# Performance work log

Hardware: AMD Instinct MI355X
Metric: run time of the kernel (lower is better)

The kernel has to match this reference:

```python
import jax, jax.numpy as jnp
import numpy as np

# dims
N = 50000      # total nodes in merged batch graph
M = 250000     # edges for GNN propagation
E = 200000     # candidate edges scored by mixture-Bernoulli head
MAXN = 512     # max_num_nodes (padded adjacency row length)
H = 128        # hidden_dim = embedding_dim = msg_dim
EF = 128       # edge_feat_dim = 2 * att_edge_dim
ATT = 128      # att_hidden_dim
K = 20         # num_mix_component
L = 3          # num_GNN_layers
S = 512        # num_subgraph
B = 16         # batch of graphs
C = 1          # num_canonical_order


def setup_inputs() -> dict:
    key = jax.random.key(0)
    ks = list(jax.random.split(key, 64))
    it = iter(ks)
    nk = lambda: next(it)
    d = {}
    d['node_feat'] = jax.random.normal(nk(), (N, MAXN), jnp.float32)
    d['edge'] = jax.random.randint(nk(), (M, 2), 0, N, dtype=jnp.int32)
    d['edge_feat'] = jax.random.normal(nk(), (M, EF), jnp.float32)
    d['node_idx_gnn'] = jax.random.randint(nk(), (E, 2), 0, N, dtype=jnp.int32)
    d['label'] = (jax.random.uniform(nk(), (E,)) < 0.1).astype(jnp.float32)
    # even sorted partition of E candidate edges into S subgraphs (all nonempty)
    d['subgraph_idx'] = ((jnp.arange(E) * S) // E).astype(jnp.int32)
    # bc_idx = repeat_interleave(arange(B*C), subgraphs_per_graph)
    d['bc_idx'] = jnp.repeat(jnp.arange(B * C, dtype=jnp.int32), S // (B * C))
    # params
    def lin(k, out_d, in_d):
        return jax.random.normal(k, (out_d, in_d), jnp.float32) * (1.0 / np.sqrt(in_d))
    d['dec_W'] = lin(nk(), H, MAXN); d['dec_b'] = jnp.zeros((H,), jnp.float32)
    d['msg_W1'] = jnp.stack([lin(nk(), H, H + EF) for _ in range(L)])
    d['msg_b1'] = jnp.zeros((L, H), jnp.float32)
    d['msg_W2'] = jnp.stack([lin(nk(), H, H) for _ in range(L)])
    d['msg_b2'] = jnp.zeros((L, H), jnp.float32)
    d['att_W1'] = jnp.stack([lin(nk(), ATT, H + EF) for _ in range(L)])
    d['att_b1'] = jnp.zeros((L, ATT), jnp.float32)
    d['att_W2'] = jnp.stack([lin(nk(), H, ATT) for _ in range(L)])
    d['att_b2'] = jnp.zeros((L, H), jnp.float32)
    d['gru_Wih'] = jnp.stack([lin(nk(), 3 * H, H) for _ in range(L)])
    d['gru_bih'] = jnp.zeros((L, 3 * H), jnp.float32)
    d['gru_Whh'] = jnp.stack([lin(nk(), 3 * H, H) for _ in range(L)])
    d['gru_bhh'] = jnp.zeros((L, 3 * H), jnp.float32)
    d['th_W1'] = lin(nk(), H, H); d['th_b1'] = jnp.zeros((H,), jnp.float32)
    d['th_W2'] = lin(nk(), H, H); d['th_b2'] = jnp.zeros((H,), jnp.float32)
    d['th_W3'] = lin(nk(), K, H); d['th_b3'] = jnp.zeros((K,), jnp.float32)
    d['al_W1'] = lin(nk(), H, H); d['al_b1'] = jnp.zeros((H,), jnp.float32)
    d['al_W2'] = lin(nk(), H, H); d['al_b2'] = jnp.zeros((H,), jnp.float32)
    d['al_W3'] = lin(nk(), K, H); d['al_b3'] = jnp.zeros((K,), jnp.float32)
    return d


def _gran_forward(node_feat, edge_feat, label, dec_W, dec_b, msg_W1, msg_b1,
                  msg_W2, msg_b2, att_W1, att_b1, att_W2, att_b2, gru_Wih,
                  gru_bih, gru_Whh, gru_bhh, th_W1, th_b1, th_W2, th_b2,
                  th_W3, th_b3, al_W1, al_b1, al_W2, al_b2, al_W3, al_b3,
                  edge, node_idx_gnn, subgraph_idx, bc_idx):
    n = node_feat.shape[0]
    # decoder_input: Linear(max_num_nodes -> embedding_dim)
    state = node_feat @ dec_W.T + dec_b  # [N, H]
    src, dst = edge[:, 0], edge[:, 1]
    for l in range(L):
        if l > 0:
            state = jax.nn.relu(state)
        # _prop: gather diff, msg MLP, sigmoid attention gate, scatter-sum, GRU
        diff = state[src] - state[dst]                       # [M, H]
        ei = jnp.concatenate([diff, edge_feat], axis=1)      # [M, H+EF]
        msg = jax.nn.relu(ei @ msg_W1[l].T + msg_b1[l]) @ msg_W2[l].T + msg_b2[l]
        att = jax.nn.sigmoid(jax.nn.relu(ei @ att_W1[l].T + att_b1[l]) @ att_W2[l].T + att_b2[l])
        agg = jax.ops.segment_sum(msg * att, dst, num_segments=n)  # [N, H]
        # torch GRUCell
        gi = agg @ gru_Wih[l].T + gru_bih[l]
        gh = state @ gru_Whh[l].T + gru_bhh[l]
        i_r, i_z, i_n = jnp.split(gi, 3, axis=-1)
        h_r, h_z, h_n = jnp.split(gh, 3, axis=-1)
        r = jax.nn.sigmoid(i_r + h_r)
        z = jax.nn.sigmoid(i_z + h_z)
        nn_ = jnp.tanh(i_n + r * h_n)
        state = (1.0 - z) * nn_ + z * state
    # mixture-Bernoulli heads on candidate-edge node-state diffs
    d2 = state[node_idx_gnn[:, 0]] - state[node_idx_gnn[:, 1]]  # [E, H]
    def mlp3(x, W1, b1, W2, b2, W3, b3):
        h = jax.nn.relu(x @ W1.T + b1)
        h = jax.nn.relu(h @ W2.T + b2)
        return h @ W3.T + b3
    log_theta = mlp3(d2, th_W1, th_b1, th_W2, th_b2, th_W3, th_b3)  # [E, K]
    log_alpha = mlp3(d2, al_W1, al_b1, al_W2, al_b2, al_W3, al_b3)  # [E, K]
    # mixture_bernoulli_loss (pos_weight = 1.0)
    y = label[:, None]
    adj_loss = jax.nn.softplus(-log_theta) + (1.0 - y) * log_theta  # BCEWithLogits, [E, K]
    const = jax.ops.segment_sum(jnp.ones((label.shape[0],), log_theta.dtype), subgraph_idx, num_segments=S)
    reduce_adj = jax.ops.segment_sum(adj_loss, subgraph_idx, num_segments=S)     # [S, K]
    reduce_la = jax.ops.segment_sum(log_alpha, subgraph_idx, num_segments=S)
    reduce_la = jax.nn.log_softmax(reduce_la / const[:, None], axis=-1)
    log_prob = jax.scipy.special.logsumexp(-reduce_adj + reduce_la, axis=1)      # [S]
    bc_log_prob = jax.ops.segment_sum(log_prob, bc_idx, num_segments=B * C)
    bc_const = jax.ops.segment_sum(const, bc_idx, num_segments=B * C)
    bc_loss = (bc_log_prob / bc_const).reshape(B, C)
    b_loss = jax.scipy.special.logsumexp(bc_loss, axis=1)  # logsumexp over orderings
    return jnp.mean(-b_loss)


def reference(node_feat, edge, edge_feat, node_idx_gnn, label, subgraph_idx,
              bc_idx, dec_W, dec_b, msg_W1, msg_b1, msg_W2, msg_b2, att_W1,
              att_b1, att_W2, att_b2, gru_Wih, gru_bih, gru_Whh, gru_bhh,
              th_W1, th_b1, th_W2, th_b2, th_W3, th_b3, al_W1, al_b1, al_W2,
              al_b2, al_W3, al_b3):
    return _gran_forward(node_feat, edge_feat, label, dec_W, dec_b, msg_W1,
                         msg_b1, msg_W2, msg_b2, att_W1, att_b1, att_W2,
                         att_b2, gru_Wih, gru_bih, gru_Whh, gru_bhh, th_W1,
                         th_b1, th_W2, th_b2, th_W3, th_b3, al_W1, al_b1,
                         al_W2, al_b2, al_W3, al_b3, edge, node_idx_gnn,
                         subgraph_idx, bc_idx)
```

## Files before the change

### kernel.cpp

```cpp
#include <hip/hip_runtime.h>
#include <cstdint>
#include <cstddef>


typedef __bf16 bf16x8 __attribute__((ext_vector_type(8)));
typedef short  s16x8  __attribute__((ext_vector_type(8)));
typedef short  s16x4  __attribute__((ext_vector_type(4)));
typedef float  f32x4  __attribute__((ext_vector_type(4)));

__device__ inline unsigned short f2bf(float f) {
    return __builtin_bit_cast(unsigned short, (__bf16)f);
}
__device__ inline float bf2f(unsigned short b) {
    return __uint_as_float(((unsigned int)b) << 16);
}
__device__ inline unsigned int pk2(float a, float b) {
    return ((unsigned int)f2bf(b) << 16) | f2bf(a);
}
__device__ inline f32x4 MFMA(bf16x8 a, bf16x8 b, f32x4 c) {
    return __builtin_amdgcn_mfma_f32_16x16x32_bf16(a, b, c, 0, 0, 0);
}

__device__ inline bf16x8 ld_swz(const char* lds, int row, int unit) {
    return *(const bf16x8*)(lds + row * 256 + ((unit ^ (row & 7)) << 4));
}
__device__ inline void hid_write(char* HID, int h0, int erow, s16x4 s4) {
    int unit = h0 >> 3;
    *(s16x4*)(HID + erow * 256 + ((unit ^ (erow & 7)) << 4) + ((h0 & 4) << 1)) = s4;
}
__device__ inline bf16x8 ldA(const short* __restrict__ Wb, int K, int row, int koff) {
    return *(const bf16x8*)(Wb + (size_t)row * K + koff);
}
__device__ inline bf16x8 ld_f32_frag(const float* __restrict__ p) {
    float4 a = *(const float4*)p, b = *(const float4*)(p + 4);
    s16x8 s;
    s[0] = f2bf(a.x); s[1] = f2bf(a.y); s[2] = f2bf(a.z); s[3] = f2bf(a.w);
    s[4] = f2bf(b.x); s[5] = f2bf(b.y); s[6] = f2bf(b.z); s[7] = f2bf(b.w);
    return __builtin_bit_cast(bf16x8, s);
}

#define NPACK 31
struct PrepackArgs {
    const float* src[NPACK];
    short*       dst[NPACK];
    int stride[NPACK];
    int rows[NPACK];
    int rowsTot[NPACK];
    int cols[NPACK];
};

__global__ void prepack(PrepackArgs a) {
    int e = blockIdx.y;
    int row = blockIdx.x;
    if (row >= a.rowsTot[e]) return;
    int c8 = threadIdx.x;
    if (c8 * 8 >= a.cols[e]) return;
    s16x8 s = {};
    if (row < a.rows[e]) {
        const float* p = a.src[e] + (size_t)row * a.stride[e] + c8 * 8;
        float4 x = *(const float4*)p, y = *(const float4*)(p + 4);
        s[0] = f2bf(x.x); s[1] = f2bf(x.y); s[2] = f2bf(x.z); s[3] = f2bf(x.w);
        s[4] = f2bf(y.x); s[5] = f2bf(y.y); s[6] = f2bf(y.z); s[7] = f2bf(y.w);
    }
    *(s16x8*)(a.dst[e] + (size_t)row * a.cols[e] + c8 * 8) = s;
}

__device__ inline void proj_gemm_store(const char* ST, char* PJ,
                                       const short* __restrict__ projW,
                                       short* __restrict__ proj,
                                       int rb, int R, int tid)
{
    const int l = tid & 63, w = tid >> 6;
    f32x4 accP[2][2][4] = {};
#pragma unroll
    for (int ks = 0; ks < 4; ++ks) {
        int koff = ks * 32 + (l >> 4) * 8;
        bf16x8 aw[2][2];
#pragma unroll
        for (int pc = 0; pc < 2; ++pc)
#pragma unroll
            for (int mt = 0; mt < 2; ++mt)
                aw[pc][mt] = ldA(projW, 128, pc * 128 + 32 * w + 16 * mt + (l & 15), koff);
#pragma unroll
        for (int n = 0; n < 4; ++n) {
            bf16x8 b = ld_swz(ST, 16 * n + (l & 15), ks * 4 + (l >> 4));
#pragma unroll
            for (int pc = 0; pc < 2; ++pc)
#pragma unroll
                for (int mt = 0; mt < 2; ++mt)
                    accP[pc][mt][n] = MFMA(aw[pc][mt], b, accP[pc][mt][n]);
        }
    }
    const int half = w >> 1;
#pragma unroll
    for (int hh = 0; hh < 2; ++hh) {
        __syncthreads();
        if (half == hh) {
#pragma unroll
            for (int pc = 0; pc < 2; ++pc)
#pragma unroll
                for (int mt = 0; mt < 2; ++mt) {
                    int h0 = 32 * w + 16 * mt + ((l >> 4) << 2);
                    int colp = 2 * h0 + 4 * pc - 128 * hh;
#pragma unroll
                    for (int n = 0; n < 4; ++n) {
                        f32x4 v = accP[pc][mt][n];
                        s16x4 s4;
                        s4[0] = f2bf(v[0]); s4[1] = f2bf(v[1]);
                        s4[2] = f2bf(v[2]); s4[3] = f2bf(v[3]);
                        hid_write(PJ, colp, 16 * n + (l & 15), s4);
                    }
                }
        }
        __syncthreads();
#pragma unroll
        for (int p2 = 0; p2 < 4; ++p2) {
            int row = p2 * 16 + (tid >> 4);
            int r = rb + row;
            if (r < R) {
                bf16x8 v = ld_swz(PJ, row, tid & 15);
                *(s16x8*)(proj + (size_t)r * 256 + hh * 128 + (tid & 15) * 8) =
                    __builtin_bit_cast(s16x8, v);
            }
        }
    }
}

__global__ __launch_bounds__(256, 3)
void dec_proj(const float* __restrict__ nf, int R,
              const short* __restrict__ decWb, const float* __restrict__ bias,
              const short* __restrict__ projW,
              short* __restrict__ sOut, short* __restrict__ proj)
{
    __shared__ char ST[16384];
    __shared__ char PJ[16384];
    const int tid = threadIdx.x, l = tid & 63, w = tid >> 6;
    const int rb = blockIdx.x * 64;

    const float* brow[4];
#pragma unroll
    for (int n = 0; n < 4; ++n) {
        int row = rb + 16 * n + (l & 15); if (row >= R) row = R - 1;
        brow[n] = nf + (size_t)row * 512;
    }

    f32x4 acc[2][4] = {};
    for (int kc = 0; kc < 512; kc += 128) {
#pragma unroll
        for (int ks = 0; ks < 4; ++ks) {
            int koff = kc + ks * 32 + (l >> 4) * 8;
            bf16x8 a0 = ldA(decWb, 512, 32 * w + (l & 15), koff);
            bf16x8 a1 = ldA(decWb, 512, 32 * w + 16 + (l & 15), koff);
#pragma unroll
            for (int n = 0; n < 4; ++n) {
                bf16x8 b = ld_f32_frag(brow[n] + koff);
                acc[0][n] = MFMA(a0, b, acc[0][n]);
                acc[1][n] = MFMA(a1, b, acc[1][n]);
            }
        }
    }
#pragma unroll
    for (int mt = 0; mt < 2; ++mt) {
        int c0 = 32 * w + 16 * mt + ((l >> 4) << 2);
        float4 bv = *(const float4*)&bias[c0];
#pragma unroll
        for (int n = 0; n < 4; ++n) {
            f32x4 v = acc[mt][n];
            s16x4 s4;
            s4[0] = f2bf(v[0] + bv.x); s4[1] = f2bf(v[1] + bv.y);
            s4[2] = f2bf(v[2] + bv.z); s4[3] = f2bf(v[3] + bv.w);
            hid_write(ST, c0, 16 * n + (l & 15), s4);
        }
    }
    __syncthreads();
#pragma unroll
    for (int p2 = 0; p2 < 4; ++p2) {
        int row = p2 * 16 + (tid >> 4);
        int r = rb + row;
        if (r < R) {
            bf16x8 v = ld_swz(ST, row, tid & 15);
            *(s16x8*)(sOut + (size_t)r * 128 + (tid & 15) * 8) =
                __builtin_bit_cast(s16x8, v);
        }
    }
    proj_gemm_store(ST, PJ, projW, proj, rb, R, tid);
}

template<int HAS_PROJ>
__global__ __launch_bounds__(256, 2)
void node_fused(const short* __restrict__ aggb, const short* __restrict__ sin_,
                const short* __restrict__ Wih, const short* __restrict__ Whh,
                const float* __restrict__ bih, const float* __restrict__ bhh,
                const short* __restrict__ projW,
                short* __restrict__ sOut, short* __restrict__ proj, int R)
{
    __shared__ char ST[16384];
    __shared__ char PJ[16384];
    const int tid = threadIdx.x, l = tid & 63, w = tid >> 6;
    const int rb = blockIdx.x * 64;

    const short* arow[4];
    const short* srow[4];
#pragma unroll
    for (int n = 0; n < 4; ++n) {
        int row = rb + 16 * n + (l & 15); if (row >= R) row = R - 1;
        arow[n] = aggb + (size_t)row * 128;
        srow[n] = sin_ + (size_t)row * 128;
    }
    s16x4 svv[2][4];
#pragma unroll
    for (int mt = 0; mt < 2; ++mt) {
        int c0 = 32 * w + 16 * mt + ((l >> 4) << 2);
#pragma unroll
        for (int n = 0; n < 4; ++n)
            svv[mt][n] = *(const s16x4*)(srow[n] + c0);
    }

    unsigned int rpk[2][4][2], zpk[2][4][2];

    for (int p = 0; p < 3; ++p) {
        f32x4 gia[2][4] = {}, gha[2][4] = {};
#pragma unroll
        for (int ks = 0; ks < 4; ++ks) {
            int koff = ks * 32 + (l >> 4) * 8;
            bf16x8 ai0 = ldA(Wih, 128, p * 128 + 32 * w + (l & 15), koff);
            bf16x8 ai1 = ldA(Wih, 128, p * 128 + 32 * w + 16 + (l & 15), koff);
            bf16x8 ah0 = ldA(Whh, 128, p * 128 + 32 * w + (l & 15), koff);
            bf16x8 ah1 = ldA(Whh, 128, p * 128 + 32 * w + 16 + (l & 15), koff);
#pragma unroll
            for (int n = 0; n < 4; ++n) {
                bf16x8 ba = *(const bf16x8*)(arow[n] + koff);
                bf16x8 bs = *(const bf16x8*)(srow[n] + koff);
                gia[0][n] = MFMA(ai0, ba, gia[0][n]);
                gia[1][n] = MFMA(ai1, ba, gia[1][n]);
                gha[0][n] = MFMA(ah0, bs, gha[0][n]);
                gha[1][n] = MFMA(ah1, bs, gha[1][n]);
            }
        }
#pragma unroll
        for (int mt = 0; mt < 2; ++mt) {
            int c0 = 32 * w + 16 * mt + ((l >> 4) << 2);
            float4 bi = *(const float4*)&bih[p * 128 + c0];
            float4 bh = *(const float4*)&bhh[p * 128 + c0];
            float biv[4] = {bi.x, bi.y, bi.z, bi.w};
            float bhv[4] = {bh.x, bh.y, bh.z, bh.w};
#pragma unroll
            for (int n = 0; n < 4; ++n) {
                float gv[4], hv[4];
#pragma unroll
                for (int q = 0; q < 4; ++q) {
                    gv[q] = gia[mt][n][q] + biv[q];
                    hv[q] = gha[mt][n][q] + bhv[q];
                }
                if (p == 0) {
                    rpk[mt][n][0] = pk2(1.f / (1.f + expf(-(gv[0] + hv[0]))),
                                        1.f / (1.f + expf(-(gv[1] + hv[1]))));
                    rpk[mt][n][1] = pk2(1.f / (1.f + expf(-(gv[2] + hv[2]))),
                                        1.f / (1.f + expf(-(gv[3] + hv[3]))));
                } else if (p == 1) {
                    zpk[mt][n][0] = pk2(1.f / (1.f + expf(-(gv[0] + hv[0]))),
                                        1.f / (1.f + expf(-(gv[1] + hv[1]))));
                    zpk[mt][n][1] = pk2(1.f / (1.f + expf(-(gv[2] + hv[2]))),
                                        1.f / (1.f + expf(-(gv[3] + hv[3]))));
                } else {
                    s16x4 s4;
#pragma unroll
                    for (int q = 0; q < 4; ++q) {
                        unsigned int ru = rpk[mt][n][q >> 1], zu = zpk[mt][n][q >> 1];
                        float r = bf2f((unsigned short)((q & 1) ? (ru >> 16) : (ru & 0xffffu)));
                        float z = bf2f((unsigned short)((q & 1) ? (zu >> 16) : (zu & 0xffffu)));
                        float nn = tanhf(gv[q] + r * hv[q]);
                        float o = (1.f - z) * nn + z * bf2f((unsigned short)svv[mt][n][q]);
                        s4[q] = f2bf(HAS_PROJ ? fmaxf(o, 0.f) : o);
                    }
                    hid_write(ST, c0, 16 * n + (l & 15), s4);
                }
            }
        }
    }
    __syncthreads();
#pragma unroll
    for (int p2 = 0; p2 < 4; ++p2) {
        int row = p2 * 16 + (tid >> 4);
        int r = rb + row;
        if (r < R) {
            bf16x8 v = ld_swz(ST, row, tid & 15);
            *(s16x8*)(sOut + (size_t)r * 128 + (tid & 15) * 8) =
                __builtin_bit_cast(s16x8, v);
        }
    }
    if (HAS_PROJ)
        proj_gemm_store(ST, PJ, projW, proj, rb, R, tid);
}

__global__ __launch_bounds__(256, 3)
void edge_fused2(const short* __restrict__ efc,
                 const int* __restrict__ srcs, const int* __restrict__ dsts,
                 const short* __restrict__ proj,
                 const short* __restrict__ mW1b, const short* __restrict__ mW2,
                 const short* __restrict__ aW1b, const short* __restrict__ aW2,
                 const float* __restrict__ mb1, const float* __restrict__ mb2,
                 const float* __restrict__ ab1, const float* __restrict__ ab2,
                 short* __restrict__ msgatt, int M, int ntiles)
{
    __shared__ char HIDm[16384];
    __shared__ char HIDa[16384];
    const int tid = threadIdx.x, l = tid & 63, w = tid >> 6;
    int q = ntiles >> 3, r = ntiles & 7;
    int xcd = blockIdx.x & 7, o = blockIdx.x >> 3;
    int tile = (xcd < r ? xcd * (q + 1) : r * (q + 1) + (xcd - r) * q) + o;
    const int pb = tile * 64;

    const char* erow[4];
    int dstv[4];
    s16x8 psv[2][4];
    {
#pragma unroll
        for (int n = 0; n < 4; ++n) {
            int pos = pb + 16 * n + (l & 15); if (pos >= M) pos = M - 1;
            int sv = srcs[pos];
            dstv[n] = dsts[pos];
            erow[n] = (const char*)(efc + (size_t)pos * 128);
#pragma unroll
            for (int mt = 0; mt < 2; ++mt) {
                int off = 2 * (32 * w + 16 * mt + ((l >> 4) << 2));
                psv[mt][n] = *(const s16x8*)(proj + (size_t)sv * 256 + off);
            }
        }
    }

    f32x4 accm[2][4] = {}, acca[2][4] = {};
#pragma unroll
    for (int ks = 0; ks < 4; ++ks) {
        int koff = ks * 32 + (l >> 4) * 8;
        bf16x8 am0 = ldA(mW1b, 128, 32 * w + (l & 15), koff);
        bf16x8 am1 = ldA(mW1b, 128, 32 * w + 16 + (l & 15), koff);
        bf16x8 aa0 = ldA(aW1b, 128, 32 * w + (l & 15), koff);
        bf16x8 aa1 = ldA(aW1b, 128, 32 * w + 16 + (l & 15), koff);
#pragma unroll
        for (int n = 0; n < 4; ++n) {
            bf16x8 b = *(const bf16x8*)(erow[n] + koff * 2);
            accm[0][n] = MFMA(am0, b, accm[0][n]);
            accm[1][n] = MFMA(am1, b, accm[1][n]);
            acca[0][n] = MFMA(aa0, b, acca[0][n]);
            acca[1][n] = MFMA(aa1, b, acca[1][n]);
        }
    }
#pragma unroll
    for (int mt = 0; mt < 2; ++mt) {
        int h0 = 32 * w + 16 * mt + ((l >> 4) << 2);
        float4 bm = *(const float4*)&mb1[h0];
        float4 ba = *(const float4*)&ab1[h0];
        float bmv[4] = {bm.x, bm.y, bm.z, bm.w};
        float bav[4] = {ba.x, ba.y, ba.z, ba.w};
#pragma unroll
        for (int n = 0; n < 4; ++n) {
            s16x8 ps = psv[mt][n];
            s16x8 pd = *(const s16x8*)(proj + (size_t)dstv[n] * 256 + 2 * h0);
            f32x4 vm = accm[mt][n], va = acca[mt][n];
            s16x4 sm, sa;
#pragma unroll
            for (int qq = 0; qq < 4; ++qq) {
                float m_ = vm[qq] + bmv[qq] + bf2f((unsigned short)ps[qq])
                           - bf2f((unsigned short)pd[qq]);
                float a_ = va[qq] + bav[qq] + bf2f((unsigned short)ps[qq + 4])
                           - bf2f((unsigned short)pd[qq + 4]);
                sm[qq] = f2bf(fmaxf(m_, 0.f));
                sa[qq] = f2bf(fmaxf(a_, 0.f));
            }
            hid_write(HIDm, h0, 16 * n + (l & 15), sm);
            hid_write(HIDa, h0, 16 * n + (l & 15), sa);
        }
    }
    __syncthreads();

    f32x4 acc2m[2][4] = {}, acc2a[2][4] = {};
#pragma unroll
    for (int ks = 0; ks < 4; ++ks) {
        int koff = ks * 32 + (l >> 4) * 8;
        bf16x8 wm0 = ldA(mW2, 128, 32 * w + (l & 15), koff);
        bf16x8 wm1 = ldA(mW2, 128, 32 * w + 16 + (l & 15), koff);
        bf16x8 wa0 = ldA(aW2, 128, 32 * w + (l & 15), koff);
        bf16x8 wa1 = ldA(aW2, 128, 32 * w + 16 + (l & 15), koff);
#pragma unroll
        for (int n = 0; n < 4; ++n) {
            bf16x8 bm = ld_swz(HIDm, 16 * n + (l & 15), ks * 4 + (l >> 4));
            bf16x8 ba = ld_swz(HIDa, 16 * n + (l & 15), ks * 4 + (l >> 4));
            acc2m[0][n] = MFMA(wm0, bm, acc2m[0][n]);
            acc2m[1][n] = MFMA(wm1, bm, acc2m[1][n]);
            acc2a[0][n] = MFMA(wa0, ba, acc2a[0][n]);
            acc2a[1][n] = MFMA(wa1, ba, acc2a[1][n]);
        }
    }
    __syncthreads();
#pragma unroll
    for (int mt = 0; mt < 2; ++mt) {
        int c0 = 32 * w + 16 * mt + ((l >> 4) << 2);
        float4 bm2 = *(const float4*)&mb2[c0];
        float4 ba2 = *(const float4*)&ab2[c0];
#pragma unroll
        for (int n = 0; n < 4; ++n) {
            f32x4 m_ = acc2m[mt][n], a_ = acc2a[mt][n];
            float o0 = (m_[0] + bm2.x) / (1.f + expf(-(a_[0] + ba2.x)));
            float o1 = (m_[1] + bm2.y) / (1.f + expf(-(a_[1] + ba2.y)));
            float o2 = (m_[2] + bm2.z) / (1.f + expf(-(a_[2] + ba2.z)));
            float o3 = (m_[3] + bm2.w) / (1.f + expf(-(a_[3] + ba2.w)));
            s16x4 s4;
            s4[0] = f2bf(o0); s4[1] = f2bf(o1); s4[2] = f2bf(o2); s4[3] = f2bf(o3);
            hid_write(HIDm, c0, 16 * n + (l & 15), s4);
        }
    }
    __syncthreads();
#pragma unroll
    for (int p2 = 0; p2 < 4; ++p2) {
        int row = p2 * 16 + (tid >> 4);
        int pos = pb + row;
        if (pos < M) {
            bf16x8 v = ld_swz(HIDm, row, tid & 15);
            *(s16x8*)(msgatt + (size_t)pos * 128 + (tid & 15) * 8) =
                __builtin_bit_cast(s16x8, v);
        }
    }
}

__global__ __launch_bounds__(256, 4)
void mlp_loss(const short* __restrict__ sP, const int* __restrict__ gidx,
              const float* __restrict__ label, const int* __restrict__ sg,
              const short* __restrict__ thW1, const short* __restrict__ thW2,
              const short* __restrict__ thW3,
              const float* __restrict__ thb1, const float* __restrict__ thb2,
              const float* __restrict__ thb3,
              const short* __restrict__ alW1, const short* __restrict__ alW2,
              const short* __restrict__ alW3,
              const float* __restrict__ alb1, const float* __restrict__ alb2,
              const float* __restrict__ alb3,
              float* __restrict__ radj, float* __restrict__ rla,
              float* __restrict__ cntS, int E, int S)
{
    __shared__ char D2T[16384];
    __shared__ char HID[16384];
    __shared__ float sacc[2][2][20];
    __shared__ float scnt[2];
    __shared__ int sbase;
    const int tid = threadIdx.x, l = tid & 63, w = tid >> 6;
    const int eb = blockIdx.x * 64;

    if (tid == 0) sbase = sg[eb];
    if (tid < 80) sacc[tid / 40][(tid / 20) & 1][tid % 20] = 0.f;

    if (w == 0) {
        int e = eb + l;
        bool valid = e < E;
        int lsv = valid ? sg[e] - sg[eb] : -1;
        unsigned long long m0 = __ballot(lsv == 0);
        unsigned long long m1 = __ballot(lsv == 1);
        if (l == 0) { scnt[0] = (float)__popcll(m0); scnt[1] = (float)__popcll(m1); }
    }

    for (int i = tid; i < 64 * 16; i += 256) {
        int row = i >> 4, u = i & 15;
        int e = eb + row; if (e >= E) e = E - 1;
        int2 ab = *(const int2*)&gidx[2 * (size_t)e];
        s16x8 x = *(const s16x8*)(sP + (size_t)ab.x * 128 + u * 8);
        s16x8 y = *(const s16x8*)(sP + (size_t)ab.y * 128 + u * 8);
        s16x8 d;
#pragma unroll
        for (int j = 0; j < 8; ++j)
            d[j] = f2bf(bf2f((unsigned short)x[j]) - bf2f((unsigned short)y[j]));
        *(s16x8*)(D2T + row * 256 + ((u ^ (row & 7)) << 4)) = d;
    }
    __syncthreads();

    for (int pass = 0; pass < 2; ++pass) {
        const short* W1 = pass ? alW1 : thW1;
        const short* W2 = pass ? alW2 : thW2;
        const short* W3 = pass ? alW3 : thW3;
        const float* b1 = pass ? alb1 : thb1;
        const float* b2 = pass ? alb2 : thb2;
        const float* b3 = pass ? alb3 : thb3;

        f32x4 acc[2][4] = {};
#pragma unroll
        for (int ks = 0; ks < 4; ++ks) {
            int koff = ks * 32 + (l >> 4) * 8;
            bf16x8 a0 = ldA(W1, 128, 32 * w + (l & 15), koff);
            bf16x8 a1 = ldA(W1, 128, 32 * w + 16 + (l & 15), koff);
#pragma unroll
            for (int n = 0; n < 4; ++n) {
                bf16x8 b = ld_swz(D2T, 16 * n + (l & 15), ks * 4 + (l >> 4));
                acc[0][n] = MFMA(a0, b, acc[0][n]);
                acc[1][n] = MFMA(a1, b, acc[1][n]);
            }
        }
        __syncthreads();
#pragma unroll
        for (int mt = 0; mt < 2; ++mt) {
            int h0 = 32 * w + 16 * mt + ((l >> 4) << 2);
            float4 bv = *(const float4*)&b1[h0];
#pragma unroll
            for (int n = 0; n < 4; ++n) {
                f32x4 v = acc[mt][n];
                s16x4 s4;
                s4[0] = f2bf(fmaxf(v[0] + bv.x, 0.f));
                s4[1] = f2bf(fmaxf(v[1] + bv.y, 0.f));
                s4[2] = f2bf(fmaxf(v[2] + bv.z, 0.f));
                s4[3] = f2bf(fmaxf(v[3] + bv.w, 0.f));
                hid_write(HID, h0, 16 * n + (l & 15), s4);
            }
        }
        __syncthreads();
        f32x4 acc2[2][4] = {};
#pragma unroll
        for (int ks = 0; ks < 4; ++ks) {
            int koff = ks * 32 + (l >> 4) * 8;
            bf16x8 a0 = ldA(W2, 128, 32 * w + (l & 15), koff);
            bf16x8 a1 = ldA(W2, 128, 32 * w + 16 + (l & 15), koff);
#pragma unroll
            for (int n = 0; n < 4; ++n) {
                bf16x8 b = ld_swz(HID, 16 * n + (l & 15), ks * 4 + (l >> 4));
                acc2[0][n] = MFMA(a0, b, acc2[0][n]);
                acc2[1][n] = MFMA(a1, b, acc2[1][n]);
            }
        }
        __syncthreads();
#pragma unroll
        for (int mt = 0; mt < 2; ++mt) {
            int h0 = 32 * w + 16 * mt + ((l >> 4) << 2);
            float4 bv = *(const float4*)&b2[h0];
#pragma unroll
            for (int n = 0; n < 4; ++n) {
                f32x4 v = acc2[mt][n];
                s16x4 s4;
                s4[0] = f2bf(fmaxf(v[0] + bv.x, 0.f));
                s4[1] = f2bf(fmaxf(v[1] + bv.y, 0.f));
                s4[2] = f2bf(fmaxf(v[2] + bv.z, 0.f));
                s4[3] = f2bf(fmaxf(v[3] + bv.w, 0.f));
                hid_write(HID, h0, 16 * n + (l & 15), s4);
            }
        }
        __syncthreads();
        f32x4 acc3[2] = {};
#pragma unroll
        for (int ks = 0; ks < 4; ++ks) {
            int koff = ks * 32 + (l >> 4) * 8;
            bf16x8 a0 = ldA(W3, 128, (l & 15), koff);
            bf16x8 a1 = ldA(W3, 128, 16 + (l & 15), koff);
            bf16x8 b = ld_swz(HID, 16 * w + (l & 15), ks * 4 + (l >> 4));
            acc3[0] = MFMA(a0, b, acc3[0]);
            acc3[1] = MFMA(a1, b, acc3[1]);
        }
        {
            int e = eb + 16 * w + (l & 15);
            bool val = e < E;
            float lsf = val ? (float)(sg[e] - sbase) : 0.f;
            float yv = (pass == 0 && val) ? label[e] : 0.f;
#pragma unroll
            for (int mt = 0; mt < 2; ++mt) {
#pragma unroll
                for (int qq = 0; qq < 4; ++qq) {
                    int k = 16 * mt + ((l >> 4) << 2) + qq;
                    bool kok = k < 20;
                    float bk = kok ? b3[k] : 0.f;
                    float vv = 0.f;
                    if (val && kok) {
                        float t = acc3[mt][qq] + bk;
                        if (pass == 0) {
                            float sp = fmaxf(-t, 0.f) + log1pf(expf(-fabsf(t)));
                            vv = sp + (1.f - yv) * t;
                        } else {
                            vv = t;
                        }
                    }
                    float vA = vv * (1.f - lsf), vB = vv * lsf;
                    vA += __shfl_xor(vA, 1); vB += __shfl_xor(vB, 1);
                    vA += __shfl_xor(vA, 2); vB += __shfl_xor(vB, 2);
                    vA += __shfl_xor(vA, 4); vB += __shfl_xor(vB, 4);
                    vA += __shfl_xor(vA, 8); vB += __shfl_xor(vB, 8);
                    if ((l & 15) == 0 && kok) {
                        atomicAdd(&sacc[pass][0][k], vA);
                        if (vB != 0.f) atomicAdd(&sacc[pass][1][k], vB);
                    }
                }
            }
        }
    }
    __syncthreads();
    if (tid < 40) {
        int ls = tid / 20, k = tid % 20;
        int s = sbase + ls;
        if (s < S) {
            float v  = sacc[0][ls][k];
            float v2 = sacc[1][ls][k];
            if (v  != 0.f) atomicAdd(&radj[s * 20 + k], v);
            if (v2 != 0.f) atomicAdd(&rla[s * 20 + k], v2);
        }
    }
    if (tid < 2) {
        int s = sbase + tid;
        if (s < S && scnt[tid] != 0.f) atomicAdd(&cntS[s], scnt[tid]);
    }
}

__global__ void csr_count(const int* __restrict__ edge, int* __restrict__ cnt, int M) {
    int e = blockIdx.x * 256 + threadIdx.x;
    if (e < M) atomicAdd(&cnt[edge[2 * (size_t)e + 1]], 1);
}

__global__ void csr_scan(const int* __restrict__ cnt, int* __restrict__ rowptr,
                         int* __restrict__ wofs, int N)
{
    __shared__ int part[1024];
    int t = threadIdx.x;
    int chunk = (N + 1023) / 1024;
    int b0 = t * chunk, b1 = b0 + chunk; if (b1 > N) b1 = N; if (b0 > N) b0 = N;
    int s = 0;
    for (int i = b0; i < b1; ++i) s += cnt[i];
    part[t] = s;
    __syncthreads();
    for (int off = 1; off < 1024; off <<= 1) {
        int v = (t >= off) ? part[t - off] : 0;
        __syncthreads();
        part[t] += v;
        __syncthreads();
    }
    int run = (t ? part[t - 1] : 0);
    for (int i = b0; i < b1; ++i) { rowptr[i] = run; wofs[i] = run; run += cnt[i]; }
    if (t == 1023) rowptr[N] = run;
}

__global__ void csr_scatter2(const int* __restrict__ edge, int* __restrict__ wofs,
                             int* __restrict__ eidx, int* __restrict__ srcs,
                             int* __restrict__ dsts, int M)
{
    int e = blockIdx.x * 256 + threadIdx.x;
    if (e < M) {
        int2 sd = *(const int2*)&edge[2 * (size_t)e];
        int p = atomicAdd(&wofs[sd.y], 1);
        eidx[p] = e; srcs[p] = sd.x; dsts[p] = sd.y;
    }
}

__global__ void ef_gather(const float* __restrict__ ef, const int* __restrict__ eidx,
                          short* __restrict__ efc, int M)
{
    long i = (long)blockIdx.x * 256 + threadIdx.x;
    if (i >= (long)M * 16) return;
    int p = (int)(i >> 4), u = (int)(i & 15);
    int e = eidx[p];
    const float* sp = ef + (size_t)e * 128 + u * 8;
    float4 a = *(const float4*)sp, b = *(const float4*)(sp + 4);
    s16x8 s;
    s[0] = f2bf(a.x); s[1] = f2bf(a.y); s[2] = f2bf(a.z); s[3] = f2bf(a.w);
    s[4] = f2bf(b.x); s[5] = f2bf(b.y); s[6] = f2bf(b.z); s[7] = f2bf(b.w);
    *(s16x8*)(efc + (size_t)p * 128 + u * 8) = s;
}

__global__ __launch_bounds__(256)
void agg_gather3(const short* __restrict__ msgatt, const int* __restrict__ rowptr,
                 short* __restrict__ aggb, int N)
{
    int wid = blockIdx.x * 4 + (threadIdx.x >> 6);
    int l = threadIdx.x & 63;
    int v = wid * 4 + (l >> 4);
    int u = l & 15;
    if (v >= N) return;
    int b = rowptr[v], e = rowptr[v + 1];
    float acc[8] = {};
    for (int i = b; i < e; ++i) {
        s16x8 x = *(const s16x8*)(msgatt + (size_t)i * 128 + u * 8);
#pragma unroll
        for (int j = 0; j < 8; ++j) acc[j] += bf2f((unsigned short)x[j]);
    }
    s16x8 o;
#pragma unroll
    for (int j = 0; j < 8; ++j) o[j] = f2bf(acc[j]);
    *(s16x8*)(aggb + (size_t)v * 128 + u * 8) = o;
}

__global__ void final_kernel(const float* __restrict__ radj, const float* __restrict__ rla,
                             const float* __restrict__ cnt, const int* __restrict__ bc_idx,
                             float* __restrict__ out)
{
    __shared__ float bcl[16], bcc[16];
    const int s = threadIdx.x;
    if (s < 16) { bcl[s] = 0.f; bcc[s] = 0.f; }
    __syncthreads();
    float c = cnt[s];
    float x[20];
    float mx = -1e30f;
#pragma unroll
    for (int k = 0; k < 20; ++k) { x[k] = rla[s * 20 + k] / c; mx = fmaxf(mx, x[k]); }
    float se = 0.f;
#pragma unroll
    for (int k = 0; k < 20; ++k) se += expf(x[k] - mx);
    float lse = mx + logf(se);
    float t[20];
    float m2 = -1e30f;
#pragma unroll
    for (int k = 0; k < 20; ++k) { t[k] = -radj[s * 20 + k] + x[k] - lse; m2 = fmaxf(m2, t[k]); }
    float s2 = 0.f;
#pragma unroll
    for (int k = 0; k < 20; ++k) s2 += expf(t[k] - m2);
    float lp = m2 + logf(s2);
    atomicAdd(&bcl[bc_idx[s]], lp);
    atomicAdd(&bcc[bc_idx[s]], c);
    __syncthreads();
    if (s == 0) {
        float a = 0.f;
        for (int b = 0; b < 16; ++b) a += bcl[b] / bcc[b];
        out[0] = -a / 16.f;
    }
}

extern "C" void kernel_launch(void* const* d_in, const int* in_sizes, int n_in,
                              void* d_out, int out_size, void* d_ws, size_t ws_size,
                              hipStream_t stream)
{
    const float* node_feat = (const float*)d_in[0];
    const int*   edge      = (const int*)  d_in[1];
    const float* edge_feat = (const float*)d_in[2];
    const int*   gnn_idx   = (const int*)  d_in[3];
    const float* label     = (const float*)d_in[4];
    const int*   sg_idx    = (const int*)  d_in[5];
    const int*   bc_idx    = (const int*)  d_in[6];
    const float* dec_W  = (const float*)d_in[7];
    const float* dec_b  = (const float*)d_in[8];
    const float* msg_W1 = (const float*)d_in[9];
    const float* msg_b1 = (const float*)d_in[10];
    const float* msg_W2 = (const float*)d_in[11];
    const float* msg_b2 = (const float*)d_in[12];
    const float* att_W1 = (const float*)d_in[13];
    const float* att_b1 = (const float*)d_in[14];
    const float* att_W2 = (const float*)d_in[15];
    const float* att_b2 = (const float*)d_in[16];
    const float* gru_Wih = (const float*)d_in[17];
    const float* gru_bih = (const float*)d_in[18];
    const float* gru_Whh = (const float*)d_in[19];
    const float* gru_bhh = (const float*)d_in[20];
    const float* th_W1 = (const float*)d_in[21];
    const float* th_b1 = (const float*)d_in[22];
    const float* th_W2 = (const float*)d_in[23];
    const float* th_b2 = (const float*)d_in[24];
    const float* th_W3 = (const float*)d_in[25];
    const float* th_b3 = (const float*)d_in[26];
    const float* al_W1 = (const float*)d_in[27];
    const float* al_b1 = (const float*)d_in[28];
    const float* al_W2 = (const float*)d_in[29];
    const float* al_b2 = (const float*)d_in[30];
    const float* al_W3 = (const float*)d_in[31];
    const float* al_b3 = (const float*)d_in[32];

    const int N = in_sizes[0] / 512;
    const int M = in_sizes[1] / 2;
    const int E = in_sizes[3] / 2;
    const int S = in_sizes[6];

    size_t off = 0;
    auto alloc = [&](size_t bytes) {
        char* p = (char*)d_ws + off;
        off += (bytes + 255) & ~(size_t)255;
        return p;
    };
    short* decWb  = (short*)alloc((size_t)128 * 512 * 2);
    short* projWb = (short*)alloc((size_t)3 * 256 * 128 * 2);
    short* mW1bB  = (short*)alloc((size_t)3 * 128 * 128 * 2);
    short* aW1bB  = (short*)alloc((size_t)3 * 128 * 128 * 2);
    short* mW2B   = (short*)alloc((size_t)3 * 128 * 128 * 2);
    short* aW2B   = (short*)alloc((size_t)3 * 128 * 128 * 2);
    short* gihB   = (short*)alloc((size_t)3 * 384 * 128 * 2);
    short* ghhB   = (short*)alloc((size_t)3 * 384 * 128 * 2);
    short* thW1B  = (short*)alloc((size_t)128 * 128 * 2);
    short* thW2B  = (short*)alloc((size_t)128 * 128 * 2);
    short* thW3B  = (short*)alloc((size_t)32 * 128 * 2);
    short* alW1B  = (short*)alloc((size_t)128 * 128 * 2);
    short* alW2B  = (short*)alloc((size_t)128 * 128 * 2);
    short* alW3B  = (short*)alloc((size_t)32 * 128 * 2);
    short* sA     = (short*)alloc((size_t)N * 128 * 2);
    short* sB     = (short*)alloc((size_t)N * 128 * 2);
    short* sP     = (short*)alloc((size_t)N * 128 * 2);
    short* efc    = (short*)alloc((size_t)M * 128 * 2);
    short* msgatt = (short*)alloc((size_t)M * 128 * 2);
    short* proj   = (short*)alloc((size_t)N * 256 * 2);
    short* aggb   = (short*)alloc((size_t)N * 128 * 2);
    int*   cntN   = (int*)  alloc((size_t)N * 4);
    int*   wofs   = (int*)  alloc((size_t)N * 4);
    int*   rowptr = (int*)  alloc((size_t)(N + 1) * 4);
    int*   eidx   = (int*)  alloc((size_t)M * 4);
    int*   srcs   = (int*)  alloc((size_t)M * 4);
    int*   dsts   = (int*)  alloc((size_t)M * 4);
    float* radj   = (float*)alloc((size_t)S * 20 * 4);
    float* rla    = (float*)alloc((size_t)S * 20 * 4);
    float* cntS   = (float*)alloc((size_t)S * 4);

    PrepackArgs pa;
    int ei = 0;
    auto add = [&](const float* s, short* d, int stride, int rows, int rowsTot, int cols) {
        pa.src[ei] = s; pa.dst[ei] = d; pa.stride[ei] = stride;
        pa.rows[ei] = rows; pa.rowsTot[ei] = rowsTot; pa.cols[ei] = cols; ++ei;
    };
    add(dec_W, decWb, 512, 128, 128, 512);
    for (int l = 0; l < 3; ++l) {
        add(msg_W1 + (size_t)l * 128 * 256,       projWb + (size_t)l * 256 * 128,          256, 128, 128, 128);
        add(att_W1 + (size_t)l * 128 * 256,       projWb + (size_t)l * 256 * 128 + 16384,  256, 128, 128, 128);
        add(msg_W1 + (size_t)l * 128 * 256 + 128, mW1bB + (size_t)l * 16384,               256, 128, 128, 128);
        add(att_W1 + (size_t)l * 128 * 256 + 128, aW1bB + (size_t)l * 16384,               256, 128, 128, 128);
        add(msg_W2 + (size_t)l * 16384,           mW2B + (size_t)l * 16384,                128, 128, 128, 128);
        add(att_W2 + (size_t)l * 16384,           aW2B + (size_t)l * 16384,                128, 128, 128, 128);
        add(gru_Wih + (size_t)l * 49152,          gihB + (size_t)l * 49152,                128, 384, 384, 128);
        add(gru_Whh + (size_t)l * 49152,          ghhB + (size_t)l * 49152,                128, 384, 384, 128);
    }
    add(th_W1, thW1B, 128, 128, 128, 128);
    add(th_W2, thW2B, 128, 128, 128, 128);
    add(th_W3, thW3B, 128, 20, 32, 128);
    add(al_W1, alW1B, 128, 128, 128, 128);
    add(al_W2, alW2B, 128, 128, 128, 128);
    add(al_W3, alW3B, 128, 20, 32, 128);

    const dim3 blk(256);
    const int gN64 = (N + 63) / 64;
    const int gE64 = (E + 63) / 64;
    const int gMt  = (M + 255) / 256;
    const int ntilesM = (M + 63) / 64;
    const int gAgg = (N + 15) / 16;

    hipMemsetAsync(radj, 0, (size_t)(S * 20 * 2 + S) * 4, stream);
    hipMemsetAsync(cntN, 0, (size_t)N * 4, stream);

    prepack<<<dim3(384, NPACK), dim3(64), 0, stream>>>(pa);

    csr_count   <<<gMt, blk, 0, stream>>>(edge, cntN, M);
    csr_scan    <<<1, 1024, 0, stream>>>(cntN, rowptr, wofs, N);
    csr_scatter2<<<gMt, blk, 0, stream>>>(edge, wofs, eidx, srcs, dsts, M);
    ef_gather   <<<(int)(((long)M * 16 + 255) / 256), blk, 0, stream>>>(edge_feat, eidx, efc, M);

    dec_proj<<<gN64, blk, 0, stream>>>(node_feat, N, decWb, dec_b, projWb, sA, proj);

    short* bufs[2] = { sA, sB };
    for (int l = 0; l < 3; ++l) {
        short* sin  = bufs[l & 1];
        short* sout = (l == 2) ? sP : bufs[(l + 1) & 1];
        edge_fused2<<<ntilesM, blk, 0, stream>>>(efc, srcs, dsts, proj,
            mW1bB + (size_t)l * 16384, mW2B + (size_t)l * 16384,
            aW1bB + (size_t)l * 16384, aW2B + (size_t)l * 16384,
            msg_b1 + l * 128, msg_b2 + l * 128,
            att_b1 + l * 128, att_b2 + l * 128,
            msgatt, M, ntilesM);
        agg_gather3<<<gAgg, blk, 0, stream>>>(msgatt, rowptr, aggb, N);
        if (l < 2) {
            node_fused<1><<<gN64, blk, 0, stream>>>(aggb, sin,
                gihB + (size_t)l * 49152, ghhB + (size_t)l * 49152,
                gru_bih + l * 384, gru_bhh + l * 384,
                projWb + (size_t)(l + 1) * 256 * 128, sout, proj, N);
        } else {
            node_fused<0><<<gN64, blk, 0, stream>>>(aggb, sin,
                gihB + (size_t)l * 49152, ghhB + (size_t)l * 49152,
                gru_bih + l * 384, gru_bhh + l * 384,
                nullptr, sout, nullptr, N);
        }
    }

    mlp_loss<<<gE64, blk, 0, stream>>>(sP, gnn_idx, label, sg_idx,
        thW1B, thW2B, thW3B, th_b1, th_b2, th_b3,
        alW1B, alW2B, alW3B, al_b1, al_b2, al_b3,
        radj, rla, cntS, E, S);
    final_kernel<<<1, S, 0, stream>>>(radj, rla, cntS, bc_idx, (float*)d_out);
}
```

Measured before the change: 1.220 ms.

## Fuse CSR message aggregation into GRU node kernel via LDS staging

Drops the separate agg_gather3 kernel and moves the per-node CSR sum of messages into the GRU node kernel. Aggregated messages and the input state are staged in swizzled LDS tiles and fed to the MFMAs from there, so the aggregate buffer never takes a global write and read-back and one launch per layer goes away. In exchange, LDS per block doubles to 64KB, which may lower occupancy. The serial gather loop also now runs inside the GEMM kernel with only 64 nodes per block, so there is less parallelism to hide gather latency.

```diff
diff --git a/kernel.cpp b/kernel.cpp
--- a/kernel.cpp
+++ b/kernel.cpp
@@ -27,6 +27,10 @@
 __device__ inline void hid_write(char* HID, int h0, int erow, s16x4 s4) {
     int unit = h0 >> 3;
     *(s16x4*)(HID + erow * 256 + ((unit ^ (erow & 7)) << 4) + ((h0 & 4) << 1)) = s4;
+}
+__device__ inline s16x4 ld_swz4(const char* lds, int row, int c0) {
+    int unit = c0 >> 3;
+    return *(const s16x4*)(lds + row * 256 + ((unit ^ (row & 7)) << 4) + ((c0 & 4) << 1));
 }
 __device__ inline bf16x8 ldA(const short* __restrict__ Wb, int K, int row, int koff) {
     return *(const bf16x8*)(Wb + (size_t)row * K + koff);
@@ -188,33 +192,42 @@
 
 template<int HAS_PROJ>
 __global__ __launch_bounds__(256, 2)
-void node_fused(const short* __restrict__ aggb, const short* __restrict__ sin_,
-                const short* __restrict__ Wih, const short* __restrict__ Whh,
-                const float* __restrict__ bih, const float* __restrict__ bhh,
-                const short* __restrict__ projW,
-                short* __restrict__ sOut, short* __restrict__ proj, int R)
-{
+void node_fused2(const short* __restrict__ msgatt, const int* __restrict__ rowptr,
+                 const short* __restrict__ sin_,
+                 const short* __restrict__ Wih, const short* __restrict__ Whh,
+                 const float* __restrict__ bih, const float* __restrict__ bhh,
+                 const short* __restrict__ projW,
+                 short* __restrict__ sOut, short* __restrict__ proj, int R)
+{
+    __shared__ char AGT[16384];
+    __shared__ char SIN[16384];
     __shared__ char ST[16384];
     __shared__ char PJ[16384];
     const int tid = threadIdx.x, l = tid & 63, w = tid >> 6;
     const int rb = blockIdx.x * 64;
 
-    const short* arow[4];
-    const short* srow[4];
-#pragma unroll
-    for (int n = 0; n < 4; ++n) {
-        int row = rb + 16 * n + (l & 15); if (row >= R) row = R - 1;
-        arow[n] = aggb + (size_t)row * 128;
-        srow[n] = sin_ + (size_t)row * 128;
-    }
-    s16x4 svv[2][4];
-#pragma unroll
-    for (int mt = 0; mt < 2; ++mt) {
-        int c0 = 32 * w + 16 * mt + ((l >> 4) << 2);
-#pragma unroll
-        for (int n = 0; n < 4; ++n)
-            svv[mt][n] = *(const s16x4*)(srow[n] + c0);
-    }
+    for (int pass = 0; pass < 4; ++pass) {
+        int row = pass * 16 + (tid >> 4);
+        int node = rb + row;
+        int u = tid & 15;
+        float acc[8] = {};
+        s16x8 sv = {};
+        if (node < R) {
+            int b = rowptr[node], e = rowptr[node + 1];
+            for (int i = b; i < e; ++i) {
+                s16x8 x = *(const s16x8*)(msgatt + (size_t)i * 128 + u * 8);
+#pragma unroll
+                for (int j = 0; j < 8; ++j) acc[j] += bf2f((unsigned short)x[j]);
+            }
+            sv = *(const s16x8*)(sin_ + (size_t)node * 128 + u * 8);
+        }
+        s16x8 o;
+#pragma unroll
+        for (int j = 0; j < 8; ++j) o[j] = f2bf(acc[j]);
+        *(s16x8*)(AGT + row * 256 + ((u ^ (row & 7)) << 4)) = o;
+        *(s16x8*)(SIN + row * 256 + ((u ^ (row & 7)) << 4)) = sv;
+    }
+    __syncthreads();
 
     unsigned int rpk[2][4][2], zpk[2][4][2];
 
@@ -229,8 +242,8 @@
             bf16x8 ah1 = ldA(Whh, 128, p * 128 + 32 * w + 16 + (l & 15), koff);
 #pragma unroll
             for (int n = 0; n < 4; ++n) {
-                bf16x8 ba = *(const bf16x8*)(arow[n] + koff);
-                bf16x8 bs = *(const bf16x8*)(srow[n] + koff);
+                bf16x8 ba = ld_swz(AGT, 16 * n + (l & 15), ks * 4 + (l >> 4));
+                bf16x8 bs = ld_swz(SIN, 16 * n + (l & 15), ks * 4 + (l >> 4));
                 gia[0][n] = MFMA(ai0, ba, gia[0][n]);
                 gia[1][n] = MFMA(ai1, ba, gia[1][n]);
                 gha[0][n] = MFMA(ah0, bs, gha[0][n]);
@@ -263,6 +276,7 @@
                     zpk[mt][n][1] = pk2(1.f / (1.f + expf(-(gv[2] + hv[2]))),
                                         1.f / (1.f + expf(-(gv[3] + hv[3]))));
                 } else {
+                    s16x4 sv = ld_swz4(SIN, 16 * n + (l & 15), c0);
                     s16x4 s4;
 #pragma unroll
                     for (int q = 0; q < 4; ++q) {
@@ -270,7 +284,7 @@
                         float r = bf2f((unsigned short)((q & 1) ? (ru >> 16) : (ru & 0xffffu)));
                         float z = bf2f((unsigned short)((q & 1) ? (zu >> 16) : (zu & 0xffffu)));
                         float nn = tanhf(gv[q] + r * hv[q]);
-                        float o = (1.f - z) * nn + z * bf2f((unsigned short)svv[mt][n][q]);
+                        float o = (1.f - z) * nn + z * bf2f((unsigned short)sv[q]);
                         s4[q] = f2bf(HAS_PROJ ? fmaxf(o, 0.f) : o);
                     }
                     hid_write(ST, c0, 16 * n + (l & 15), s4);
@@ -653,28 +667,6 @@
     s[0] = f2bf(a.x); s[1] = f2bf(a.y); s[2] = f2bf(a.z); s[3] = f2bf(a.w);
     s[4] = f2bf(b.x); s[5] = f2bf(b.y); s[6] = f2bf(b.z); s[7] = f2bf(b.w);
     *(s16x8*)(efc + (size_t)p * 128 + u * 8) = s;
-}
-
-__global__ __launch_bounds__(256)
-void agg_gather3(const short* __restrict__ msgatt, const int* __restrict__ rowptr,
-                 short* __restrict__ aggb, int N)
-{
-    int wid = blockIdx.x * 4 + (threadIdx.x >> 6);
-    int l = threadIdx.x & 63;
-    int v = wid * 4 + (l >> 4);
-    int u = l & 15;
-    if (v >= N) return;
-    int b = rowptr[v], e = rowptr[v + 1];
-    float acc[8] = {};
-    for (int i = b; i < e; ++i) {
-        s16x8 x = *(const s16x8*)(msgatt + (size_t)i * 128 + u * 8);
-#pragma unroll
-        for (int j = 0; j < 8; ++j) acc[j] += bf2f((unsigned short)x[j]);
-    }
-    s16x8 o;
-#pragma unroll
-    for (int j = 0; j < 8; ++j) o[j] = f2bf(acc[j]);
-    *(s16x8*)(aggb + (size_t)v * 128 + u * 8) = o;
 }
 
 __global__ void final_kernel(const float* __restrict__ radj, const float* __restrict__ rla,
@@ -781,7 +773,6 @@
     short* efc    = (short*)alloc((size_t)M * 128 * 2);
     short* msgatt = (short*)alloc((size_t)M * 128 * 2);
     short* proj   = (short*)alloc((size_t)N * 256 * 2);
-    short* aggb   = (short*)alloc((size_t)N * 128 * 2);
     int*   cntN   = (int*)  alloc((size_t)N * 4);
     int*   wofs   = (int*)  alloc((size_t)N * 4);
     int*   rowptr = (int*)  alloc((size_t)(N + 1) * 4);
@@ -821,7 +812,6 @@
     const int gE64 = (E + 63) / 64;
     const int gMt  = (M + 255) / 256;
     const int ntilesM = (M + 63) / 64;
-    const int gAgg = (N + 15) / 16;
 
     hipMemsetAsync(radj, 0, (size_t)(S * 20 * 2 + S) * 4, stream);
     hipMemsetAsync(cntN, 0, (size_t)N * 4, stream);
@@ -845,14 +835,13 @@
             msg_b1 + l * 128, msg_b2 + l * 128,
             att_b1 + l * 128, att_b2 + l * 128,
             msgatt, M, ntilesM);
-        agg_gather3<<<gAgg, blk, 0, stream>>>(msgatt, rowptr, aggb, N);
         if (l < 2) {
-            node_fused<1><<<gN64, blk, 0, stream>>>(aggb, sin,
+            node_fused2<1><<<gN64, blk, 0, stream>>>(msgatt, rowptr, sin,
                 gihB + (size_t)l * 49152, ghhB + (size_t)l * 49152,
                 gru_bih + l * 384, gru_bhh + l * 384,
                 projWb + (size_t)(l + 1) * 256 * 128, sout, proj, N);
         } else {
-            node_fused<0><<<gN64, blk, 0, stream>>>(aggb, sin,
+            node_fused2<0><<<gN64, blk, 0, stream>>>(msgatt, rowptr, sin,
                 gihB + (size_t)l * 49152, ghhB + (size_t)l * 49152,
                 gru_bih + l * 384, gru_bhh + l * 384,
                 nullptr, sout, nullptr, N);
```

After: 1.194 ms. 1.02x faster.
